# Performance work log

Measured on AMD Instinct MI355X. Metric: run time of the kernel, lower is better.

Reference implementation:

```python
import jax, jax.numpy as jnp
import numpy as np

N, B, S, A, H, E = 8, 8192, 64, 16, 512, 4  # agents, batch, state, action, hidden, heads
D = H // E  # attend_dim


def setup_inputs() -> dict:
    key = jax.random.key(0)
    ks = jax.random.split(key, 12)
    g = lambda k, shape, fan: (jax.random.normal(k, shape, jnp.float32) / np.float32(np.sqrt(fan)))
    return {
        "states": jax.random.normal(ks[0], (N, B, S), jnp.float32),
        "actions": jax.random.normal(ks[1], (N, B, A), jnp.float32),
        # per-agent state encoder (Linear + LeakyReLU)
        "Ws": g(ks[2], (N, S, H), S), "bs": jnp.zeros((N, H), jnp.float32),
        # per-agent state-action encoder
        "Wsa": g(ks[3], (N, S + A, H), S + A), "bsa": jnp.zeros((N, H), jnp.float32),
        # shared per-head extractors (key/selector bias-free, value has bias+LeakyReLU)
        "Wk": g(ks[4], (E, H, D), H),
        "Wsel": g(ks[5], (E, H, D), H),
        "Wv": g(ks[6], (E, H, D), H), "bv": jnp.zeros((E, D), jnp.float32),
        # per-agent critic head (2H -> H -> 1)
        "Wc1": g(ks[7], (N, 2 * H, H), 2 * H), "bc1": jnp.zeros((N, H), jnp.float32),
        "Wc2": g(ks[8], (N, H, 1), H), "bc2": jnp.zeros((N, 1), jnp.float32),
        # per-agent value head (2H -> H -> 1)
        "Wv1": g(ks[9], (N, 2 * H, H), 2 * H), "bv1": jnp.zeros((N, H), jnp.float32),
        "Wv2": g(ks[10], (N, H, 1), H), "bv2": jnp.zeros((N, 1), jnp.float32),
    }


def reference(states, actions, Ws, bs, Wsa, bsa, Wk, Wsel, Wv, bv,
              Wc1, bc1, Wc2, bc2, Wv1, bv1, Wv2, bv2):
    lrelu = jax.nn.leaky_relu  # slope 0.01, matches nn.LeakyReLU default
    # encoders: [N,B,H]
    s_enc = lrelu(jnp.einsum('nbs,nsh->nbh', states, Ws) + bs[:, None, :])
    sa = jnp.concatenate([states, actions], axis=-1)
    sa_enc = lrelu(jnp.einsum('nbi,nih->nbh', sa, Wsa) + bsa[:, None, :])
    # per-head keys/selectors/values: [B,E,N,D]
    keys = jnp.einsum('nbh,ehd->bend', sa_enc, Wk)
    sels = jnp.einsum('nbh,ehd->bend', sa_enc, Wsel)
    vals = lrelu(jnp.einsum('nbh,ehd->bend', sa_enc, Wv) + bv[None, :, None, :])
    # each agent i attends over all agents j (including itself; no mask in source)
    logits = jnp.einsum('beid,bejd->beij', sels, keys) / jnp.float32(np.sqrt(D))
    weights = jax.nn.softmax(logits, axis=-1)
    other = jnp.einsum('beij,bejd->beid', weights, vals)  # [B,E,N,D]
    other = jnp.transpose(other, (2, 0, 1, 3)).reshape(N, B, H)  # heads concat -> [N,B,H]
    critic_in = jnp.concatenate([sa_enc, other], axis=-1)  # [N,B,2H]
    value_in = jnp.concatenate([s_enc, other], axis=-1)
    q = jnp.einsum('nbh,nho->nbo', lrelu(jnp.einsum('nbi,nih->nbh', critic_in, Wc1) + bc1[:, None, :]), Wc2) + bc2[:, None, :]
    v = jnp.einsum('nbh,nho->nbo', lrelu(jnp.einsum('nbi,nih->nbh', value_in, Wv1) + bv1[:, None, :]), Wv2) + bv2[:, None, :]
    return q, v  # each [N,B,1]
```

## Files before the change

kernel.cpp:

```cpp
#include <hip/hip_runtime.h>


#define DEVI __device__ __forceinline__

typedef unsigned short us16;
typedef __bf16 bf16x8 __attribute__((ext_vector_type(8)));
typedef float f32x4 __attribute__((ext_vector_type(4)));
typedef unsigned short u16x8 __attribute__((ext_vector_type(8)));

DEVI us16 f2bf(float f) {
  unsigned u = __builtin_bit_cast(unsigned, f);
  u += 0x7FFFu + ((u >> 16) & 1u);
  return (us16)(u >> 16);
}
DEVI float bf2f(us16 h) {
  unsigned u = ((unsigned)h) << 16;
  return __builtin_bit_cast(float, u);
}
DEVI float lrelu(float v) { return v > 0.f ? v : 0.01f * v; }
DEVI int pk2(float a, float b) { return (int)f2bf(a) | ((int)f2bf(b) << 16); }

DEVI void gload16(const us16* g, us16* l) {
  __builtin_amdgcn_global_load_lds(
      (const __attribute__((address_space(1))) void*)g,
      (__attribute__((address_space(3))) void*)l, 16, 0, 0);
}

__global__ void tconv_k(const float* __restrict__ src, long srcSlice, int K, int O,
                        us16* __restrict__ dst, long dstSlice, int dstRowOff,
                        int ldd, int Kpad)
{
  __shared__ float t[32][33];
  const int s = blockIdx.z;
  const int k0 = blockIdx.x * 32, o0 = blockIdx.y * 32;
  const int lx = threadIdx.x, ly = threadIdx.y;
#pragma unroll
  for (int i = 0; i < 4; i++) {
    int k = k0 + ly + i * 8, o = o0 + lx;
    float v = 0.f;
    if (k < K && o < O) v = src[(long)s * srcSlice + (long)k * O + o];
    t[ly + i * 8][lx] = v;
  }
  __syncthreads();
#pragma unroll
  for (int i = 0; i < 4; i++) {
    int o = o0 + ly + i * 8, k = k0 + lx;
    if (o < O && k < Kpad)
      dst[(long)s * dstSlice + (long)(dstRowOff + o) * ldd + k] = f2bf(t[lx][ly + i * 8]);
  }
}

enum { ASRC_F32 = 2, ASRC_F32_CAT = 3 };

template <int ASRC, int KTOT>
__global__ __launch_bounds__(256, 4)
void enc_gemm_k(const float* __restrict__ Ap, long aSlice,
                const float* __restrict__ A2p, long a2Slice,
                const us16* __restrict__ Btp, long bSlice,
                const float* __restrict__ bias, long biasSlice,
                us16* __restrict__ outB, long outSlice, long outRow)
{
  __shared__ us16 lA[128 * 32];
  __shared__ us16 lB[128 * 32];
  const int tid = threadIdx.x;
  const int z = blockIdx.z;
  const int m0 = blockIdx.x * 128;
  const int n0 = blockIdx.y * 128;
  const int wv = tid >> 6, lane = tid & 63;
  const int wm = (wv >> 1) * 64, wn = (wv & 1) * 64;
  const int fr = lane & 15, fk = (lane >> 4) * 8;
  const int rbase = (lane >> 4) * 4;
  const int grow = tid >> 2, gcol = (tid & 3) * 8;

  f32x4 acc[4][4];
#pragma unroll
  for (int i = 0; i < 4; i++)
#pragma unroll
    for (int j = 0; j < 4; j++) acc[i][j] = f32x4{0.f, 0.f, 0.f, 0.f};

  const us16* bbase = Btp + (long)z * bSlice + (long)n0 * KTOT;

  for (int k0 = 0; k0 < KTOT; k0 += 32) {
    int4 ra0, ra1;
    {
      const int srow = tid >> 1, scol0 = (tid & 1) * 16;
      const int kg = k0 + scol0;
      const float* a = nullptr;
      if constexpr (ASRC == ASRC_F32) {
        a = Ap + (long)z * aSlice + (long)(m0 + srow) * 64 + kg;
      } else {
        if (kg < 64)      a = Ap + (long)z * aSlice + (long)(m0 + srow) * 64 + kg;
        else if (kg < 80) a = A2p + (long)z * a2Slice + (long)(m0 + srow) * 16 + (kg - 64);
      }
      float4 f0, f1, f2, f3;
      if (a) { const float4* ap = (const float4*)a; f0 = ap[0]; f1 = ap[1]; f2 = ap[2]; f3 = ap[3]; }
      else   { f0 = make_float4(0.f, 0.f, 0.f, 0.f); f1 = f0; f2 = f0; f3 = f0; }
      ra0.x = pk2(f0.x, f0.y); ra0.y = pk2(f0.z, f0.w); ra0.z = pk2(f1.x, f1.y); ra0.w = pk2(f1.z, f1.w);
      ra1.x = pk2(f2.x, f2.y); ra1.y = pk2(f2.z, f2.w); ra1.z = pk2(f3.x, f3.y); ra1.w = pk2(f3.z, f3.w);
    }

    __syncthreads();
    {
      const us16* bb = bbase + k0 + gcol;
      gload16(bb + (long)grow * KTOT, &lB[tid * 8]);
      gload16(bb + (long)(64 + grow) * KTOT, &lB[2048 + tid * 8]);
    }
    {
      const int srow = tid >> 1, scol0 = (tid & 1) * 16;
      *(int4*)&lA[srow * 32 + scol0]     = ra0;
      *(int4*)&lA[srow * 32 + scol0 + 8] = ra1;
    }
    __syncthreads();

    bf16x8 af[4], bfg[4];
#pragma unroll
    for (int f = 0; f < 4; f++) af[f]  = *(const bf16x8*)&lA[(wm + f * 16 + fr) * 32 + fk];
#pragma unroll
    for (int f = 0; f < 4; f++) bfg[f] = *(const bf16x8*)&lB[(wn + f * 16 + fr) * 32 + fk];
#pragma unroll
    for (int fm = 0; fm < 4; fm++)
#pragma unroll
      for (int fn = 0; fn < 4; fn++)
        acc[fm][fn] = __builtin_amdgcn_mfma_f32_16x16x32_bf16(af[fm], bfg[fn], acc[fm][fn], 0, 0, 0);
  }

#pragma unroll
  for (int fm = 0; fm < 4; fm++) {
#pragma unroll
    for (int fn = 0; fn < 4; fn++) {
      int col = n0 + wn + fn * 16 + fr;
      float badd = bias[(long)z * biasSlice + col];
      us16* op = outB + (long)z * outSlice + (long)(m0 + wm + fm * 16 + rbase) * outRow + col;
#pragma unroll
      for (int j = 0; j < 4; j++) {
        float v = lrelu(acc[fm][fn][j] + badd);
        op[(long)j * outRow] = f2bf(v);
      }
    }
  }
}

enum { EPI_KSV = 1, EPI_DOT = 2 };

template <bool CAT, int KTOT>
DEVI void stage_tile(const us16* __restrict__ Ap, long aSlice,
                     const us16* __restrict__ A2p, long a2Slice,
                     const us16* __restrict__ bbase, int z, int m0, int k0,
                     int tid, us16* ldsA, us16* ldsB)
{
#pragma unroll
  for (int i = 0; i < 4; i++) {
    const int c = i * 256 + tid;
    const int r = c >> 3;
    const int col = ((c & 7) ^ (r & 7)) << 3;
    const us16* a;
    if constexpr (!CAT) {
      a = Ap + (long)z * aSlice + (long)(m0 + r) * KTOT + (k0 + col);
    } else {
      const int kg = k0 + col;
      a = (kg < 512) ? Ap  + (long)z * aSlice  + (long)(m0 + r) * 512 + kg
                     : A2p + (long)z * a2Slice + (long)(m0 + r) * 512 + (kg - 512);
    }
    gload16(a, ldsA + c * 8);
  }
#pragma unroll
  for (int i = 0; i < 4; i++) {
    const int c = i * 256 + tid;
    const int r = c >> 3;
    const int col = ((c & 7) ^ (r & 7)) << 3;
    gload16(bbase + (long)r * KTOT + (k0 + col), ldsB + c * 8);
  }
}

template <bool CAT, int EPI, int KTOT>
__global__ __launch_bounds__(256, 2)
void gemm64db_k(const us16* __restrict__ Ap, long aSlice,
                const us16* __restrict__ A2p, long a2Slice,
                const us16* __restrict__ Btp, long bSlice,
                const float* __restrict__ bias,
                us16* __restrict__ outB, long outSlice, long outRow,
                const float* __restrict__ dotW, float* __restrict__ partial)
{
  __shared__ us16 lds[2][2][128 * 64];
  const int tid = threadIdx.x;
  const int z = blockIdx.z;
  const int m0 = blockIdx.x * 128;
  const int n0 = blockIdx.y * 128;
  const int wv = tid >> 6, lane = tid & 63;
  const int wm = (wv >> 1) * 64, wn = (wv & 1) * 64;
  const int fr = lane & 15, fk = (lane >> 4) * 8;
  const int rbase = (lane >> 4) * 4;
  const int xorkey = (fr & 7) << 3;

  f32x4 acc[4][4];
#pragma unroll
  for (int i = 0; i < 4; i++)
#pragma unroll
    for (int j = 0; j < 4; j++) acc[i][j] = f32x4{0.f, 0.f, 0.f, 0.f};

  const us16* bbase = Btp + (long)z * bSlice + (long)n0 * KTOT;

  constexpr int NT = KTOT / 64;
  stage_tile<CAT, KTOT>(Ap, aSlice, A2p, a2Slice, bbase, z, m0, 0, tid,
                        &lds[0][0][0], &lds[0][1][0]);

#pragma unroll 2
  for (int t = 0; t < NT; ++t) {
    const int d = t & 1;
    if (t + 1 < NT) {
      stage_tile<CAT, KTOT>(Ap, aSlice, A2p, a2Slice, bbase, z, m0, (t + 1) * 64,
                            tid, &lds[d ^ 1][0][0], &lds[d ^ 1][1][0]);
      asm volatile("s_waitcnt vmcnt(8)" ::: "memory");
    } else {
      asm volatile("s_waitcnt vmcnt(0)" ::: "memory");
    }
    __builtin_amdgcn_s_barrier();
    __builtin_amdgcn_sched_barrier(0);

    const us16* la = &lds[d][0][0];
    const us16* lb = &lds[d][1][0];
    bf16x8 af[2][4], bfg[2][4];
#pragma unroll
    for (int ks = 0; ks < 2; ks++) {
      const int kc = ks * 32 + fk;
#pragma unroll
      for (int f = 0; f < 4; f++)
        af[ks][f]  = *(const bf16x8*)&la[(wm + f * 16 + fr) * 64 + (kc ^ xorkey)];
#pragma unroll
      for (int f = 0; f < 4; f++)
        bfg[ks][f] = *(const bf16x8*)&lb[(wn + f * 16 + fr) * 64 + (kc ^ xorkey)];
    }
    __builtin_amdgcn_s_setprio(1);
#pragma unroll
    for (int ks = 0; ks < 2; ks++)
#pragma unroll
      for (int fm = 0; fm < 4; fm++)
#pragma unroll
        for (int fn = 0; fn < 4; fn++)
          acc[fm][fn] = __builtin_amdgcn_mfma_f32_16x16x32_bf16(af[ks][fm], bfg[ks][fn], acc[fm][fn], 0, 0, 0);
    __builtin_amdgcn_s_setprio(0);
    __builtin_amdgcn_s_barrier();
    __builtin_amdgcn_sched_barrier(0);
  }

  if constexpr (EPI == EPI_DOT) {
    const float* bsl = bias + (long)z * 512;
    const float* wsl = dotW + (long)z * 512;
#pragma unroll
    for (int fm = 0; fm < 4; fm++) {
#pragma unroll
      for (int j = 0; j < 4; j++) {
        float p = 0.f;
#pragma unroll
        for (int fn = 0; fn < 4; fn++) {
          int col = n0 + wn + fn * 16 + fr;
          float v = acc[fm][fn][j] + bsl[col];
          v = lrelu(v);
          p += v * wsl[col];
        }
        p += __shfl_xor(p, 1); p += __shfl_xor(p, 2); p += __shfl_xor(p, 4); p += __shfl_xor(p, 8);
        if (fr == 0) {
          long row = (long)z * 8192 + (m0 + wm + fm * 16 + rbase + j);
          partial[row * 8 + blockIdx.y * 2 + (wv & 1)] = p;
        }
      }
    }
  } else {
#pragma unroll
    for (int fm = 0; fm < 4; fm++) {
#pragma unroll
      for (int fn = 0; fn < 4; fn++) {
        int col = n0 + wn + fn * 16 + fr;
        float badd = 0.f; bool act = false;
        if (col >= 256) { badd = bias[col - 256]; act = true; }
        us16* op = outB + (long)z * outSlice + (long)(m0 + wm + fm * 16 + rbase) * outRow + col;
#pragma unroll
        for (int j = 0; j < 4; j++) {
          float v = acc[fm][fn][j] + badd;
          if (act) v = lrelu(v);
          op[(long)j * outRow] = f2bf(v);
        }
      }
    }
  }
}

__global__ __launch_bounds__(256, 2)
void attn_k(const us16* __restrict__ ksv, us16* __restrict__ other, int e)
{
  __shared__ us16 t[4][8 * 392];
  const int wv = threadIdx.x >> 6, lane = threadIdx.x & 63;
  const long b = (long)blockIdx.x * 4 + wv;
  const us16* src = ksv + b * 3072;
#pragma unroll
  for (int i = 0; i < 6; i++) {
    int c = i * 64 + lane;
    int r = c / 48, cc = c - r * 48;
    *(int4*)&t[wv][r * 392 + cc * 8] = *(const int4*)&src[c * 8];
  }
  __syncthreads();
  const int i = lane >> 3, j = lane & 7;
  const us16* selp = &t[wv][i * 392 + 128];
  const us16* keyp = &t[wv][j * 392];
  float acc = 0.f;
#pragma unroll
  for (int d = 0; d < 128; d += 8) {
    u16x8 s8 = *(const u16x8*)&selp[d];
    u16x8 k8 = *(const u16x8*)&keyp[d];
#pragma unroll
    for (int q = 0; q < 8; q++) acc += bf2f(s8[q]) * bf2f(k8[q]);
  }
  acc *= 0.088388347648318447f;
  float mx = acc;
  mx = fmaxf(mx, __shfl_xor(mx, 1)); mx = fmaxf(mx, __shfl_xor(mx, 2)); mx = fmaxf(mx, __shfl_xor(mx, 4));
  float ex = __expf(acc - mx);
  float sm = ex;
  sm += __shfl_xor(sm, 1); sm += __shfl_xor(sm, 2); sm += __shfl_xor(sm, 4);
  float wsm = ex / sm;
  float wj[8];
  const int ibase = lane & 56;
#pragma unroll
  for (int jj = 0; jj < 8; jj++) wj[jj] = __shfl(wsm, ibase + jj);
  const int dbase = (lane & 7) * 16;
  float o[16];
#pragma unroll
  for (int q = 0; q < 16; q++) o[q] = 0.f;
#pragma unroll
  for (int jj = 0; jj < 8; jj++) {
    u16x8 v0 = *(const u16x8*)&t[wv][jj * 392 + 256 + dbase];
    u16x8 v1 = *(const u16x8*)&t[wv][jj * 392 + 256 + dbase + 8];
    float wgt = wj[jj];
#pragma unroll
    for (int q = 0; q < 8; q++) { o[q] += wgt * bf2f(v0[q]); o[8 + q] += wgt * bf2f(v1[q]); }
  }
  u16x8 r0, r1;
#pragma unroll
  for (int q = 0; q < 8; q++) { r0[q] = f2bf(o[q]); r1[q] = f2bf(o[8 + q]); }
  us16* dst = other + ((long)i * 8192 + b) * 512 + e * 128 + dbase;
  *(u16x8*)&dst[0] = r0;
  *(u16x8*)&dst[8] = r1;
}

__global__ void reduce_dot_k(const float* __restrict__ part, const float* __restrict__ b2,
                             float* __restrict__ out)
{
  int r = blockIdx.x * 256 + threadIdx.x;
  const float4* p = (const float4*)(part + (long)r * 8);
  float4 a = p[0], b = p[1];
  out[r] = b2[r >> 13] + ((a.x + a.y) + (a.z + a.w)) + ((b.x + b.y) + (b.z + b.w));
}

extern "C" void kernel_launch(void* const* d_in, const int* in_sizes, int n_in,
                              void* d_out, int out_size, void* d_ws, size_t ws_size,
                              hipStream_t stream)
{
  const float* states = (const float*)d_in[0];
  const float* actions= (const float*)d_in[1];
  const float* Ws  = (const float*)d_in[2];
  const float* bs  = (const float*)d_in[3];
  const float* Wsa = (const float*)d_in[4];
  const float* bsa = (const float*)d_in[5];
  const float* Wk  = (const float*)d_in[6];
  const float* Wsel= (const float*)d_in[7];
  const float* Wv  = (const float*)d_in[8];
  const float* bv  = (const float*)d_in[9];
  const float* Wc1 = (const float*)d_in[10];
  const float* bc1 = (const float*)d_in[11];
  const float* Wc2 = (const float*)d_in[12];
  const float* bc2 = (const float*)d_in[13];
  const float* Wv1 = (const float*)d_in[14];
  const float* bv1 = (const float*)d_in[15];
  const float* Wv2 = (const float*)d_in[16];
  const float* bv2 = (const float*)d_in[17];

  char* ws = (char*)d_ws;
  constexpr size_t OFF_WST   = 0;
  constexpr size_t OFF_WSAT  = OFF_WST   + (size_t)8 * 512 * 64 * 2;
  constexpr size_t OFF_WKVST = OFF_WSAT  + (size_t)8 * 512 * 96 * 2;
  constexpr size_t OFF_WC1T  = OFF_WKVST + (size_t)4 * 384 * 512 * 2;
  constexpr size_t OFF_WV1T  = OFF_WC1T  + (size_t)8 * 512 * 1024 * 2;
  constexpr size_t OFF_ENC   = OFF_WV1T  + (size_t)8 * 512 * 1024 * 2;
  constexpr size_t OFF_OTHER = OFF_ENC   + (size_t)8 * 8192 * 512 * 2;
  constexpr size_t OFF_KSV   = OFF_OTHER + (size_t)8 * 8192 * 512 * 2;
  constexpr size_t OFF_PART  = OFF_KSV   + (size_t)8192 * 8 * 384 * 2;
  constexpr size_t NEED      = OFF_PART  + (size_t)65536 * 8 * 4;
  if (ws_size < NEED) return;

  us16* WST   = (us16*)(ws + OFF_WST);
  us16* WSAT  = (us16*)(ws + OFF_WSAT);
  us16* WKVST = (us16*)(ws + OFF_WKVST);
  us16* WC1T  = (us16*)(ws + OFF_WC1T);
  us16* WV1T  = (us16*)(ws + OFF_WV1T);
  us16* ENC   = (us16*)(ws + OFF_ENC);
  us16* OTHER = (us16*)(ws + OFF_OTHER);
  us16* KSV   = (us16*)(ws + OFF_KSV);
  float* PART = (float*)(ws + OFF_PART);

  dim3 tb(32, 8);
  tconv_k<<<dim3(2, 16, 8),  tb, 0, stream>>>(Ws,  (long)64 * 512,  64,  512, WST,  (long)512 * 64,  0,   64,   64);
  tconv_k<<<dim3(3, 16, 8),  tb, 0, stream>>>(Wsa, (long)80 * 512,  80,  512, WSAT, (long)512 * 96,  0,   96,   96);
  tconv_k<<<dim3(16, 4, 4),  tb, 0, stream>>>(Wk,  (long)512 * 128, 512, 128, WKVST,(long)384 * 512, 0,   512,  512);
  tconv_k<<<dim3(16, 4, 4),  tb, 0, stream>>>(Wsel,(long)512 * 128, 512, 128, WKVST,(long)384 * 512, 128, 512,  512);
  tconv_k<<<dim3(16, 4, 4),  tb, 0, stream>>>(Wv,  (long)512 * 128, 512, 128, WKVST,(long)384 * 512, 256, 512,  512);
  tconv_k<<<dim3(32, 16, 8), tb, 0, stream>>>(Wc1, (long)1024 * 512,1024,512, WC1T, (long)512 * 1024,0,   1024, 1024);
  tconv_k<<<dim3(32, 16, 8), tb, 0, stream>>>(Wv1, (long)1024 * 512,1024,512, WV1T, (long)512 * 1024,0,   1024, 1024);

  enc_gemm_k<ASRC_F32_CAT, 96><<<dim3(64, 4, 8), 256, 0, stream>>>(
      states, (long)8192 * 64, actions, (long)8192 * 16, WSAT, (long)512 * 96, bsa, 512,
      ENC, (long)8192 * 512, 512);

  for (int e = 0; e < 4; e++) {
    gemm64db_k<false, EPI_KSV, 512><<<dim3(64, 3, 8), 256, 0, stream>>>(
        ENC, (long)8192 * 512, nullptr, 0, WKVST + (size_t)e * 384 * 512, 0, bv + e * 128,
        KSV, 384, 3072, nullptr, nullptr);
    attn_k<<<dim3(2048), 256, 0, stream>>>(KSV, OTHER, e);
  }

  gemm64db_k<true, EPI_DOT, 1024><<<dim3(64, 4, 8), 256, 0, stream>>>(
      ENC, (long)8192 * 512, OTHER, (long)8192 * 512, WC1T, (long)512 * 1024, bc1,
      nullptr, 0, 0, Wc2, PART);
  reduce_dot_k<<<dim3(256), 256, 0, stream>>>(PART, bc2, (float*)d_out);

  enc_gemm_k<ASRC_F32, 64><<<dim3(64, 4, 8), 256, 0, stream>>>(
      states, (long)8192 * 64, nullptr, 0, WST, (long)512 * 64, bs, 512,
      ENC, (long)8192 * 512, 512);

  gemm64db_k<true, EPI_DOT, 1024><<<dim3(64, 4, 8), 256, 0, stream>>>(
      ENC, (long)8192 * 512, OTHER, (long)8192 * 512, WV1T, (long)512 * 1024, bv1,
      nullptr, 0, 0, Wv2, PART);
  reduce_dot_k<<<dim3(256), 256, 0, stream>>>(PART, bv2, (float*)d_out + 65536);
}
```

Measured before the change: 458.9 us.

## Shrink GEMM K-tile to 32 for higher occupancy and merge weight transposes

The double-buffered MFMA GEMM now stages K-tiles of 32 instead of 64. That halves LDS use per block (32KB instead of 64KB), so launch bounds can rise to 4 blocks per CU, and the LDS swizzle is adjusted to the narrower rows. The last K-tile is peeled out of the loop so the loop body needs no branch. Separately, the five weight-transpose launches for the key/selector/value and critic/value-head weights become two launches. Smaller K-tiles mean twice as many barriers and less MFMA work per sync, and 4 blocks per CU limits registers per thread, which could cause spills with 64 fp32 accumulators.

After: 445.1 us. 1.03x faster.

```diff
diff --git a/kernel.cpp b/kernel.cpp
--- a/kernel.cpp
+++ b/kernel.cpp
@@ -48,6 +48,44 @@
     if (o < O && k < Kpad)
       dst[(long)s * dstSlice + (long)(dstRowOff + o) * ldd + k] = f2bf(t[lx][ly + i * 8]);
   }
+}
+
+__global__ void tconv3_k(const float* __restrict__ wk, const float* __restrict__ wsel,
+                         const float* __restrict__ wv, us16* __restrict__ dst)
+{
+  __shared__ float t[32][33];
+  const int zz = blockIdx.z;
+  const int e = zz & 3, m = zz >> 2;
+  const float* src = ((m == 0) ? wk : (m == 1) ? wsel : wv) + (long)e * 512 * 128;
+  us16* d = dst + (long)e * 384 * 512 + (long)(m * 128) * 512;
+  const int k0 = blockIdx.x * 32, o0 = blockIdx.y * 32;
+  const int lx = threadIdx.x, ly = threadIdx.y;
+#pragma unroll
+  for (int i = 0; i < 4; i++)
+    t[ly + i * 8][lx] = src[(long)(k0 + ly + i * 8) * 128 + (o0 + lx)];
+  __syncthreads();
+#pragma unroll
+  for (int i = 0; i < 4; i++)
+    d[(long)(o0 + ly + i * 8) * 512 + (k0 + lx)] = f2bf(t[lx][ly + i * 8]);
+}
+
+__global__ void tconvC_k(const float* __restrict__ c1, const float* __restrict__ v1,
+                         us16* __restrict__ dc, us16* __restrict__ dv)
+{
+  __shared__ float t[32][33];
+  const int zz = blockIdx.z;
+  const int n = zz & 7, m = zz >> 3;
+  const float* src = ((m == 0) ? c1 : v1) + (long)n * 1024 * 512;
+  us16* dst = ((m == 0) ? dc : dv) + (long)n * 512 * 1024;
+  const int k0 = blockIdx.x * 32, o0 = blockIdx.y * 32;
+  const int lx = threadIdx.x, ly = threadIdx.y;
+#pragma unroll
+  for (int i = 0; i < 4; i++)
+    t[ly + i * 8][lx] = src[(long)(k0 + ly + i * 8) * 512 + (o0 + lx)];
+  __syncthreads();
+#pragma unroll
+  for (int i = 0; i < 4; i++)
+    dst[(long)(o0 + ly + i * 8) * 1024 + (k0 + lx)] = f2bf(t[lx][ly + i * 8]);
 }
 
 enum { ASRC_F32 = 2, ASRC_F32_CAT = 3 };
@@ -143,16 +181,16 @@
 enum { EPI_KSV = 1, EPI_DOT = 2 };
 
 template <bool CAT, int KTOT>
-DEVI void stage_tile(const us16* __restrict__ Ap, long aSlice,
-                     const us16* __restrict__ A2p, long a2Slice,
-                     const us16* __restrict__ bbase, int z, int m0, int k0,
-                     int tid, us16* ldsA, us16* ldsB)
-{
-#pragma unroll
-  for (int i = 0; i < 4; i++) {
+DEVI void stage32(const us16* __restrict__ Ap, long aSlice,
+                  const us16* __restrict__ A2p, long a2Slice,
+                  const us16* __restrict__ bbase, int z, int m0, int k0,
+                  int tid, us16* ldsA, us16* ldsB)
+{
+#pragma unroll
+  for (int i = 0; i < 2; i++) {
     const int c = i * 256 + tid;
-    const int r = c >> 3;
-    const int col = ((c & 7) ^ (r & 7)) << 3;
+    const int r = c >> 2;
+    const int col = ((c & 3) ^ ((r >> 1) & 3)) << 3;
     const us16* a;
     if constexpr (!CAT) {
       a = Ap + (long)z * aSlice + (long)(m0 + r) * KTOT + (k0 + col);
@@ -164,24 +202,24 @@
     gload16(a, ldsA + c * 8);
   }
 #pragma unroll
-  for (int i = 0; i < 4; i++) {
+  for (int i = 0; i < 2; i++) {
     const int c = i * 256 + tid;
-    const int r = c >> 3;
-    const int col = ((c & 7) ^ (r & 7)) << 3;
+    const int r = c >> 2;
+    const int col = ((c & 3) ^ ((r >> 1) & 3)) << 3;
     gload16(bbase + (long)r * KTOT + (k0 + col), ldsB + c * 8);
   }
 }
 
 template <bool CAT, int EPI, int KTOT>
-__global__ __launch_bounds__(256, 2)
-void gemm64db_k(const us16* __restrict__ Ap, long aSlice,
+__global__ __launch_bounds__(256, 4)
+void gemm32db_k(const us16* __restrict__ Ap, long aSlice,
                 const us16* __restrict__ A2p, long a2Slice,
                 const us16* __restrict__ Btp, long bSlice,
                 const float* __restrict__ bias,
                 us16* __restrict__ outB, long outSlice, long outRow,
                 const float* __restrict__ dotW, float* __restrict__ partial)
 {
-  __shared__ us16 lds[2][2][128 * 64];
+  __shared__ us16 lds[2][2][128 * 32];
   const int tid = threadIdx.x;
   const int z = blockIdx.z;
   const int m0 = blockIdx.x * 128;
@@ -190,7 +228,7 @@
   const int wm = (wv >> 1) * 64, wn = (wv & 1) * 64;
   const int fr = lane & 15, fk = (lane >> 4) * 8;
   const int rbase = (lane >> 4) * 4;
-  const int xorkey = (fr & 7) << 3;
+  const int xorkey = ((fr >> 1) & 3) << 3;
 
   f32x4 acc[4][4];
 #pragma unroll
@@ -200,47 +238,56 @@
 
   const us16* bbase = Btp + (long)z * bSlice + (long)n0 * KTOT;
 
-  constexpr int NT = KTOT / 64;
-  stage_tile<CAT, KTOT>(Ap, aSlice, A2p, a2Slice, bbase, z, m0, 0, tid,
-                        &lds[0][0][0], &lds[0][1][0]);
+  constexpr int NT = KTOT / 32;
+  stage32<CAT, KTOT>(Ap, aSlice, A2p, a2Slice, bbase, z, m0, 0, tid,
+                     &lds[0][0][0], &lds[0][1][0]);
 
 #pragma unroll 2
-  for (int t = 0; t < NT; ++t) {
+  for (int t = 0; t < NT - 1; ++t) {
     const int d = t & 1;
-    if (t + 1 < NT) {
-      stage_tile<CAT, KTOT>(Ap, aSlice, A2p, a2Slice, bbase, z, m0, (t + 1) * 64,
-                            tid, &lds[d ^ 1][0][0], &lds[d ^ 1][1][0]);
-      asm volatile("s_waitcnt vmcnt(8)" ::: "memory");
-    } else {
-      asm volatile("s_waitcnt vmcnt(0)" ::: "memory");
-    }
+    stage32<CAT, KTOT>(Ap, aSlice, A2p, a2Slice, bbase, z, m0, (t + 1) * 32,
+                       tid, &lds[d ^ 1][0][0], &lds[d ^ 1][1][0]);
+    asm volatile("s_waitcnt vmcnt(4)" ::: "memory");
     __builtin_amdgcn_s_barrier();
     __builtin_amdgcn_sched_barrier(0);
 
     const us16* la = &lds[d][0][0];
     const us16* lb = &lds[d][1][0];
-    bf16x8 af[2][4], bfg[2][4];
-#pragma unroll
-    for (int ks = 0; ks < 2; ks++) {
-      const int kc = ks * 32 + fk;
-#pragma unroll
-      for (int f = 0; f < 4; f++)
-        af[ks][f]  = *(const bf16x8*)&la[(wm + f * 16 + fr) * 64 + (kc ^ xorkey)];
-#pragma unroll
-      for (int f = 0; f < 4; f++)
-        bfg[ks][f] = *(const bf16x8*)&lb[(wn + f * 16 + fr) * 64 + (kc ^ xorkey)];
-    }
+    bf16x8 af[4], bfg[4];
+#pragma unroll
+    for (int f = 0; f < 4; f++)
+      af[f]  = *(const bf16x8*)&la[(wm + f * 16 + fr) * 32 + (fk ^ xorkey)];
+#pragma unroll
+    for (int f = 0; f < 4; f++)
+      bfg[f] = *(const bf16x8*)&lb[(wn + f * 16 + fr) * 32 + (fk ^ xorkey)];
     __builtin_amdgcn_s_setprio(1);
 #pragma unroll
-    for (int ks = 0; ks < 2; ks++)
-#pragma unroll
-      for (int fm = 0; fm < 4; fm++)
-#pragma unroll
-        for (int fn = 0; fn < 4; fn++)
-          acc[fm][fn] = __builtin_amdgcn_mfma_f32_16x16x32_bf16(af[ks][fm], bfg[ks][fn], acc[fm][fn], 0, 0, 0);
+    for (int fm = 0; fm < 4; fm++)
+#pragma unroll
+      for (int fn = 0; fn < 4; fn++)
+        acc[fm][fn] = __builtin_amdgcn_mfma_f32_16x16x32_bf16(af[fm], bfg[fn], acc[fm][fn], 0, 0, 0);
     __builtin_amdgcn_s_setprio(0);
     __builtin_amdgcn_s_barrier();
     __builtin_amdgcn_sched_barrier(0);
+  }
+  {
+    asm volatile("s_waitcnt vmcnt(0)" ::: "memory");
+    __builtin_amdgcn_s_barrier();
+    __builtin_amdgcn_sched_barrier(0);
+    const us16* la = &lds[(NT - 1) & 1][0][0];
+    const us16* lb = &lds[(NT - 1) & 1][1][0];
+    bf16x8 af[4], bfg[4];
+#pragma unroll
+    for (int f = 0; f < 4; f++)
+      af[f]  = *(const bf16x8*)&la[(wm + f * 16 + fr) * 32 + (fk ^ xorkey)];
+#pragma unroll
+    for (int f = 0; f < 4; f++)
+      bfg[f] = *(const bf16x8*)&lb[(wn + f * 16 + fr) * 32 + (fk ^ xorkey)];
+#pragma unroll
+    for (int fm = 0; fm < 4; fm++)
+#pragma unroll
+      for (int fn = 0; fn < 4; fn++)
+        acc[fm][fn] = __builtin_amdgcn_mfma_f32_16x16x32_bf16(af[fm], bfg[fn], acc[fm][fn], 0, 0, 0);
   }
 
   if constexpr (EPI == EPI_DOT) {
@@ -397,26 +444,23 @@
   float* PART = (float*)(ws + OFF_PART);
 
   dim3 tb(32, 8);
-  tconv_k<<<dim3(2, 16, 8),  tb, 0, stream>>>(Ws,  (long)64 * 512,  64,  512, WST,  (long)512 * 64,  0,   64,   64);
-  tconv_k<<<dim3(3, 16, 8),  tb, 0, stream>>>(Wsa, (long)80 * 512,  80,  512, WSAT, (long)512 * 96,  0,   96,   96);
-  tconv_k<<<dim3(16, 4, 4),  tb, 0, stream>>>(Wk,  (long)512 * 128, 512, 128, WKVST,(long)384 * 512, 0,   512,  512);
-  tconv_k<<<dim3(16, 4, 4),  tb, 0, stream>>>(Wsel,(long)512 * 128, 512, 128, WKVST,(long)384 * 512, 128, 512,  512);
-  tconv_k<<<dim3(16, 4, 4),  tb, 0, stream>>>(Wv,  (long)512 * 128, 512, 128, WKVST,(long)384 * 512, 256, 512,  512);
-  tconv_k<<<dim3(32, 16, 8), tb, 0, stream>>>(Wc1, (long)1024 * 512,1024,512, WC1T, (long)512 * 1024,0,   1024, 1024);
-  tconv_k<<<dim3(32, 16, 8), tb, 0, stream>>>(Wv1, (long)1024 * 512,1024,512, WV1T, (long)512 * 1024,0,   1024, 1024);
+  tconv_k <<<dim3(2, 16, 8),  tb, 0, stream>>>(Ws,  (long)64 * 512, 64, 512, WST,  (long)512 * 64, 0, 64, 64);
+  tconv_k <<<dim3(3, 16, 8),  tb, 0, stream>>>(Wsa, (long)80 * 512, 80, 512, WSAT, (long)512 * 96, 0, 96, 96);
+  tconv3_k<<<dim3(16, 4, 12), tb, 0, stream>>>(Wk, Wsel, Wv, WKVST);
+  tconvC_k<<<dim3(32, 16, 16),tb, 0, stream>>>(Wc1, Wv1, WC1T, WV1T);
 
   enc_gemm_k<ASRC_F32_CAT, 96><<<dim3(64, 4, 8), 256, 0, stream>>>(
       states, (long)8192 * 64, actions, (long)8192 * 16, WSAT, (long)512 * 96, bsa, 512,
       ENC, (long)8192 * 512, 512);
 
   for (int e = 0; e < 4; e++) {
-    gemm64db_k<false, EPI_KSV, 512><<<dim3(64, 3, 8), 256, 0, stream>>>(
+    gemm32db_k<false, EPI_KSV, 512><<<dim3(64, 3, 8), 256, 0, stream>>>(
         ENC, (long)8192 * 512, nullptr, 0, WKVST + (size_t)e * 384 * 512, 0, bv + e * 128,
         KSV, 384, 3072, nullptr, nullptr);
     attn_k<<<dim3(2048), 256, 0, stream>>>(KSV, OTHER, e);
   }
 
-  gemm64db_k<true, EPI_DOT, 1024><<<dim3(64, 4, 8), 256, 0, stream>>>(
+  gemm32db_k<true, EPI_DOT, 1024><<<dim3(64, 4, 8), 256, 0, stream>>>(
       ENC, (long)8192 * 512, OTHER, (long)8192 * 512, WC1T, (long)512 * 1024, bc1,
       nullptr, 0, 0, Wc2, PART);
   reduce_dot_k<<<dim3(256), 256, 0, stream>>>(PART, bc2, (float*)d_out);
@@ -425,7 +469,7 @@
       states, (long)8192 * 64, nullptr, 0, WST, (long)512 * 64, bs, 512,
       ENC, (long)8192 * 512, 512);
 
-  gemm64db_k<true, EPI_DOT, 1024><<<dim3(64, 4, 8), 256, 0, stream>>>(
+  gemm32db_k<true, EPI_DOT, 1024><<<dim3(64, 4, 8), 256, 0, stream>>>(
       ENC, (long)8192 * 512, OTHER, (long)8192 * 512, WV1T, (long)512 * 1024, bv1,
       nullptr, 0, 0, Wv2, PART);
   reduce_dot_k<<<dim3(256), 256, 0, stream>>>(PART, bv2, (float*)d_out + 65536);
```
